# Kernel tuning notes

Measured on AMD Instinct MI355X. Metric: run time of the kernel, lower is better.

The kernel has to match this reference:

```python
import jax, jax.numpy as jnp
import numpy as np

# Dimensions (see shape_source): n_head == M == 8 is required by the module's own reshapes.
H = 8       # n_head
M = 8       # hardcoded M (must equal n_head)
D = 1024    # input_dim
E = 1024    # embed_dim
V = 128     # v_dim = embed_dim // n_head
KD = 128    # k_dim = v_dim
S = 10      # global seq_len == n_query (forced by delta_proj in-features)
K = 3       # K_num sampling points
HI, WI = 16, 16   # h_img, w_img feature-map size
BN = 4      # batch_n = batch_size // (h*w)
B = BN * HI * WI  # 1024
BNM = BN * M      # 32


def setup_inputs() -> dict:
    key = jax.random.key(0)
    ks = jax.random.split(key, 7)
    sc = 0.02
    return {
        "q": jax.random.normal(ks[0], (B, S, D), jnp.float32),
        "Wq": jax.random.normal(ks[1], (H, D, KD), jnp.float32) * sc,
        "Wk": jax.random.normal(ks[2], (H, D, KD), jnp.float32) * sc,
        "Wv": jax.random.normal(ks[3], (H, D, V * K), jnp.float32) * sc,
        "Wo": jax.random.normal(ks[4], (H, V, E), jnp.float32) * sc,
        "dw": jax.random.normal(ks[5], (2 * K * S, V * S), jnp.float32) * 0.01,
        "db": jax.random.uniform(ks[6], (2 * K * S,), jnp.float32, -1.0, 1.0),
    }


def _grid_sample_bilinear(feats, gx, gy):
    # Replicates F.grid_sample(mode='bilinear', padding_mode='zeros', align_corners=False)
    # feats: (N, h, w, S, V); gx, gy: (N, h, w, S, K) normalized grid coords in [-1, 1]-space
    n, h, w = feats.shape[0], feats.shape[1], feats.shape[2]
    ix = ((gx + 1.0) * w - 1.0) * 0.5  # unnormalize, align_corners=False
    iy = ((gy + 1.0) * h - 1.0) * 0.5
    x0 = jnp.floor(ix); y0 = jnp.floor(iy)
    x1 = x0 + 1.0;      y1 = y0 + 1.0
    wx1 = ix - x0; wx0 = 1.0 - wx1
    wy1 = iy - y0; wy0 = 1.0 - wy1
    b_idx = jnp.arange(n)[:, None, None, None, None]
    s_idx = jnp.arange(feats.shape[3])[None, None, None, :, None]

    def corner(xc, yc, wgt):
        xi = jnp.clip(xc.astype(jnp.int32), 0, w - 1)
        yi = jnp.clip(yc.astype(jnp.int32), 0, h - 1)
        valid = (xc >= 0) & (xc <= w - 1) & (yc >= 0) & (yc <= h - 1)
        val = feats[b_idx, yi, xi, s_idx]  # (N, h, w, S, K, V)
        return val * (wgt * valid)[..., None]

    return (corner(x0, y0, wx0 * wy0) + corner(x1, y0, wx1 * wy0)
            + corner(x0, y1, wx0 * wy1) + corner(x1, y1, wx1 * wy1))


def _l2norm_dim1(x):
    # F.normalize(x, p=2, dim=1) with eps=1e-12 (normalizes over the h axis)
    n = jnp.sqrt(jnp.sum(x * x, axis=1, keepdims=True))
    return x / jnp.maximum(n, 1e-12)


def _forward(q, Wq, Wk, Wv, Wo, dw, db):
    hf = q.reshape(-1, D)                                    # [B*S, D] (h defaults to q)
    qp = jnp.einsum('nd,hdk->hnk', hf, Wq).reshape(H, B, S, KD)
    kp = jnp.einsum('nd,hdk->hnk', hf, Wk).reshape(H, B, S, KD)
    vp = jnp.einsum('nd,hdk->hnk', hf, Wv).reshape(H, B, S * K, V)

    # torch: q.permute(1,2,3,0).contiguous().view(H, B, -1)  (memory reinterpretation)
    q2 = jnp.transpose(qp, (1, 2, 3, 0)).reshape(H, B, S * KD)

    deltas = (q2 @ dw.T + db).reshape(BNM, HI, WI, S, K, 2)

    gy, gx = jnp.meshgrid(jnp.arange(HI) / (HI - 1), jnp.arange(WI) / (WI - 1), indexing='ij')
    ref = jnp.stack((gx, gy), axis=-1).astype(q.dtype)        # (h, w, 2)

    pd = ref[None, :, :, None, None, :] + deltas              # (BNM, h, w, S, K, 2)
    vgx = _l2norm_dim1(pd[..., 0])
    vgy = _l2norm_dim1(pd[..., 1])

    feats = kp.reshape(BNM, HI, WI, S, V)                     # torch view of (H,B,S,k)
    samp = _grid_sample_bilinear(feats, vgx, vgy)             # (BNM, h, w, S, K, V)
    # torch stacks loop results at index k*S + s on a trailing dim, then permutes channels last
    samp = jnp.transpose(samp, (0, 1, 2, 4, 3, 5)).reshape(BNM, HI, WI, K * S, V)
    k_attn = samp.reshape(M, B, K * S, V)

    q_attn = q2.reshape(M, B, S, V)
    qk = jnp.einsum('mbqv,mbkv->mbqk', q_attn, k_attn) * (1.0 / np.sqrt(KD))
    attn = jax.nn.softmax(qk, axis=-1)                        # (M, B, S, K*S)
    attn_map = attn.mean(axis=0)[:, 0]                        # (B, K*S)

    head = jnp.einsum('mbqk,mbkv->mbqv', attn, vp)            # (M, B, S, V)
    head_flat = jnp.transpose(head, (1, 2, 0, 3)).reshape(B * S, H * V)
    out = (head_flat @ Wo.reshape(H * V, E)).reshape(B, S, E)
    return out, attn_map


def reference(q, Wq, Wk, Wv, Wo, dw, db):
    return _forward(q, Wq, Wk, Wv, Wo, dw, db)
```

## Files before the change

kernel.cpp:

```cpp
#include <hip/hip_runtime.h>


typedef float    f32x4 __attribute__((ext_vector_type(4)));
typedef short    s16x8 __attribute__((ext_vector_type(8)));
typedef unsigned short u16x8 __attribute__((ext_vector_type(8)));
typedef unsigned short u16;

__device__ __forceinline__ u16 f2bf(float f) {
  union { float f; unsigned u; } x; x.f = f;
  unsigned r = x.u + 0x7FFFu + ((x.u >> 16) & 1u);
  return (u16)(r >> 16);
}
__device__ __forceinline__ float bf2f(u16 u) {
  union { unsigned u; float f; } x; x.u = ((unsigned)u) << 16;
  return x.f;
}

#define ASYNC16(g, l) __builtin_amdgcn_global_load_lds(                       \
    (const __attribute__((address_space(1))) void*)(g),                       \
    (__attribute__((address_space(3))) void*)(l), 16, 0, 0)
#define WAITV(n) asm volatile("s_waitcnt vmcnt(" #n ")" ::: "memory")
#define WAITL    asm volatile("s_waitcnt lgkmcnt(0)" ::: "memory")
#define SB       __builtin_amdgcn_sched_barrier(0)
#define BAR      __builtin_amdgcn_s_barrier()

__global__ __launch_bounds__(256) void conv_all(
    const float* __restrict__ q, const float* __restrict__ Wq,
    const float* __restrict__ Wk, const float* __restrict__ Wv,
    const float* __restrict__ Wo, const float* __restrict__ dw,
    u16* __restrict__ Abf, u16* __restrict__ Wcat, u16* __restrict__ dwbf)
{
  int bid = blockIdx.x;
  if (bid < 5120) {
    int i = bid * 256 + threadIdx.x;
    const float4* s = (const float4*)q + (size_t)i * 2;
    float4 a = s[0], b = s[1];
    u16x8 o;
    o[0] = f2bf(a.x); o[1] = f2bf(a.y); o[2] = f2bf(a.z); o[3] = f2bf(a.w);
    o[4] = f2bf(b.x); o[5] = f2bf(b.y); o[6] = f2bf(b.z); o[7] = f2bf(b.w);
    *(u16x8*)(Abf + (size_t)i * 8) = o;
  } else if (bid < 8192) {
    int i = (bid - 5120) * 256 + threadIdx.x;
    int c = i >> 7;
    int d0 = (i & 127) * 8;
    const float* src; int stride;
    if (c < 1024)      { int kq = c >> 3, h = c & 7;
                         src = Wq + (size_t)h * 131072 + kq;      stride = 128; }
    else if (c < 2048) { int j = c - 1024; int h = j >> 7, k = j & 127;
                         src = Wk + (size_t)h * 131072 + k;       stride = 128; }
    else if (c < 5120) { int j = c - 2048; int h = j / 384, cc = j - h * 384;
                         src = Wv + (size_t)h * 393216 + cc;      stride = 384; }
    else               { int e = c - 5120;
                         src = Wo + e;                            stride = 1024; }
    u16x8 o;
#pragma unroll
    for (int r = 0; r < 8; ++r) o[r] = f2bf(src[(size_t)(d0 + r) * stride]);
    *(u16x8*)(Wcat + (size_t)c * 1024 + d0) = o;
  } else {
    int i = (bid - 8192) * 256 + threadIdx.x;
    if (i >= 10240) return;
    int row = i / 160, ch = i - row * 160;
    int srow = (row < 60) ? row : 0;
    const float4* s = (const float4*)(dw + (size_t)srow * 1280 + ch * 8);
    float4 a = s[0], b = s[1];
    u16x8 o;
    o[0] = f2bf(a.x); o[1] = f2bf(a.y); o[2] = f2bf(a.z); o[3] = f2bf(a.w);
    o[4] = f2bf(b.x); o[5] = f2bf(b.y); o[6] = f2bf(b.z); o[7] = f2bf(b.w);
    *(u16x8*)(dwbf + (size_t)row * 1280 + ch * 8) = o;
  }
}

__global__ __launch_bounds__(512, 2) void gemm_320(
    const u16* __restrict__ base, long bOff, u16* __restrict__ C, int ldc)
{
  extern __shared__ __align__(16) char smem[];
  const int tid = threadIdx.x;
  const int l   = tid & 63;
  const int wid = tid >> 6;
  const int wm  = wid >> 2;
  const int wn  = wid & 3;
  const int row0 = blockIdx.x * 320;
  const int col0 = blockIdx.y * 320;

  int eoff[5];
#pragma unroll
  for (int j = 0; j < 5; ++j) {
    int c = j * 512 + tid;
    int mc = (c < 1280) ? c : c - 1280;
    int rp = mc >> 3, s = mc & 7, gs = s ^ (rp & 7);
    int grow = rp * 2 + (gs >> 2), gk = (gs & 3) * 8;
    eoff[j] = (c < 1280) ? ((row0 + grow) * 1024 + gk)
                         : (int)(bOff + (size_t)(col0 + grow) * 1024 + gk);
  }

#define STG320(tt, bb) do {                                                   \
    _Pragma("unroll")                                                         \
    for (int j_ = 0; j_ < 5; ++j_)                                            \
      ASYNC16(base + eoff[j_] + (tt) * 32,                                    \
              smem + (bb) * 40960 + (j_ * 512 + tid) * 16);                   \
  } while (0)

  const int lrow = l & 15, lk = l >> 4;
  int aoff[10], boff[5];
  {
    int rowA = wm * 160 + lrow;
    int rpA = rowA >> 1, odA = (rowA & 1) << 2;
#pragma unroll
    for (int fm = 0; fm < 10; ++fm) {
      int rp = rpA + fm * 8;
      aoff[fm] = rp * 128 + (((odA | lk) ^ (rp & 7)) * 16);
    }
    int rowB = wn * 80 + lrow;
    int rpB = rowB >> 1, odB = (rowB & 1) << 2;
#pragma unroll
    for (int fn = 0; fn < 5; ++fn) {
      int rp = rpB + fn * 8;
      boff[fn] = 20480 + rp * 128 + (((odB | lk) ^ (rp & 7)) * 16);
    }
  }

  f32x4 acc[10][5];
#pragma unroll
  for (int i = 0; i < 10; ++i)
#pragma unroll
    for (int j = 0; j < 5; ++j) acc[i][j] = (f32x4){0.f, 0.f, 0.f, 0.f};

  STG320(0, 0); STG320(1, 1);
  WAITV(5);
  SB; BAR; SB;

  for (int t = 0; t < 32; ++t) {
    const int cb = t % 3;
    if (t + 2 < 32) STG320(t + 2, (t + 2) % 3);
    const char* Ab = smem + cb * 40960;
    s16x8 bR[5];
#pragma unroll
    for (int fn = 0; fn < 5; ++fn) bR[fn] = *(const s16x8*)(Ab + boff[fn]);
#pragma unroll
    for (int fm = 0; fm < 10; ++fm) {
      s16x8 aT = *(const s16x8*)(Ab + aoff[fm]);
#pragma unroll
      for (int fn = 0; fn < 5; ++fn)
        acc[fm][fn] = __builtin_amdgcn_mfma_f32_16x16x32_bf16(
            aT, bR[fn], acc[fm][fn], 0, 0, 0);
    }
    if (t + 2 < 32) { WAITV(5); }
    else if (t == 30) { WAITV(0); }
    SB; BAR; SB;
  }
#undef STG320

  const int crow = l >> 4, ccol = l & 15;
#pragma unroll
  for (int fm = 0; fm < 10; ++fm)
#pragma unroll
    for (int fn = 0; fn < 5; ++fn) {
      size_t rb = (size_t)(row0 + wm * 160 + fm * 16 + crow * 4);
      int col = col0 + wn * 80 + fn * 16 + ccol;
#pragma unroll
      for (int r = 0; r < 4; ++r)
        C[(rb + r) * ldc + col] = f2bf(acc[fm][fn][r]);
    }
}

template<int OUTBF>
__global__ __launch_bounds__(512, 2) void gemm_256(
    const u16* __restrict__ A, const u16* __restrict__ Bt,
    void* __restrict__ Cv, int ldc)
{
  extern __shared__ __align__(16) char smem[];
  const int tid = threadIdx.x;
  const int l   = tid & 63;
  const int wid = tid >> 6;
  const int wm  = wid >> 2;
  const int wn  = wid & 3;
  const int row0 = blockIdx.x * 256;
  const int col0 = blockIdx.y * 256;

  size_t goff[2]; int doff[2];
#pragma unroll
  for (int j = 0; j < 2; ++j) {
    int c = j * 512 + tid;
    int drow = c >> 3;
    int sg = (c & 7) ^ (drow & 7);
    goff[j] = (size_t)(drow * 2 + (sg >> 2)) * 1024 + (sg & 3) * 8;
    doff[j] = c * 16;
  }
  const u16* Agb = A  + (size_t)row0 * 1024;
  const u16* Bgb = Bt + (size_t)col0 * 1024;

#define STG(mtx, kh, tt, dd) do {                                             \
    const u16* sb_ = (mtx) ? Bgb : Agb;                                       \
    char* lb_ = smem + ((mtx) ? 65536 : 0) + (dd) * 32768 + (kh) * 16384;     \
    ASYNC16(sb_ + goff[0] + (tt) * 64 + (kh) * 32, lb_ + doff[0]);            \
    ASYNC16(sb_ + goff[1] + (tt) * 64 + (kh) * 32, lb_ + doff[1]);            \
  } while (0)

  const int lrow = l & 15, lk = l >> 4;
  const int p = (((lrow & 1) << 2) | lk) ^ ((lrow >> 1) & 7);
  const int rofs = (lrow >> 1) * 128 + p * 16;

  f32x4 acc[8][4];
#pragma unroll
  for (int i = 0; i < 8; ++i)
#pragma unroll
    for (int j = 0; j < 4; ++j) acc[i][j] = (f32x4){0.f, 0.f, 0.f, 0.f};

  STG(0, 0, 0, 0); STG(1, 0, 0, 0);
  STG(0, 1, 0, 0); STG(1, 1, 0, 0);
  WAITV(4);
  BAR; SB;

  for (int t = 0; t < 16; ++t) {
    const int d = t & 1;
    const char* Abase = smem + d * 32768;
    const char* Bbase = smem + 65536 + d * 32768;
    s16x8 aR[8], bR[4];

#pragma unroll
    for (int kh = 0; kh < 2; ++kh) {
      const char* Ab = Abase + kh * 16384 + wm * 8192;
      const char* Bb = Bbase + kh * 16384 + wn * 4096;
#pragma unroll
      for (int fm = 0; fm < 4; ++fm)
        aR[fm] = *(const s16x8*)(Ab + fm * 1024 + rofs);
#pragma unroll
      for (int fn = 0; fn < 4; ++fn)
        bR[fn] = *(const s16x8*)(Bb + fn * 1024 + rofs);
      if (t < 15) STG(0, kh, t + 1, d ^ 1);
      SB; BAR;
      WAITL; SB;
      __builtin_amdgcn_s_setprio(1);
#pragma unroll
      for (int fm = 0; fm < 4; ++fm)
#pragma unroll
        for (int fn = 0; fn < 4; ++fn)
          acc[fm][fn] = __builtin_amdgcn_mfma_f32_16x16x32_bf16(
              aR[fm], bR[fn], acc[fm][fn], 0, 0, 0);
      __builtin_amdgcn_s_setprio(0);
      SB; BAR;

#pragma unroll
      for (int fm = 4; fm < 8; ++fm)
        aR[fm] = *(const s16x8*)(Ab + fm * 1024 + rofs);
      if (t < 15) STG(1, kh, t + 1, d ^ 1);
      SB; BAR;
      WAITL; SB;
      __builtin_amdgcn_s_setprio(1);
#pragma unroll
      for (int fm = 4; fm < 8; ++fm)
#pragma unroll
        for (int fn = 0; fn < 4; ++fn)
          acc[fm][fn] = __builtin_amdgcn_mfma_f32_16x16x32_bf16(
              aR[fm], bR[fn], acc[fm][fn], 0, 0, 0);
      __builtin_amdgcn_s_setprio(0);
      if (kh == 0) {
        if (t == 15) WAITV(0); else WAITV(4);
      } else {
        if (t < 15) WAITV(4);
      }
      SB; BAR;
    }
  }
#undef STG

  const int crow = l >> 4, ccol = l & 15;
#pragma unroll
  for (int fm = 0; fm < 8; ++fm)
#pragma unroll
    for (int fn = 0; fn < 4; ++fn) {
      size_t rb = (size_t)(row0 + wm * 128 + fm * 16 + crow * 4);
      int col = col0 + wn * 64 + fn * 16 + ccol;
      if (OUTBF) {
        u16* Cq = (u16*)Cv;
#pragma unroll
        for (int r = 0; r < 4; ++r)
          Cq[(rb + r) * ldc + col] = f2bf(acc[fm][fn][r]);
      } else {
        float* Cf = (float*)Cv;
#pragma unroll
        for (int r = 0; r < 4; ++r)
          Cf[(rb + r) * ldc + col] = acc[fm][fn][r];
      }
    }
}

__global__ __launch_bounds__(256) void delta_mfma(
    const u16* __restrict__ proj, const u16* __restrict__ dwbf,
    const float* __restrict__ db, float* __restrict__ deltas)
{
  __shared__ __align__(16) u16 As[4][64 * 32];
  __shared__ __align__(16) u16 Bs[4][64 * 32];
  const int tid  = threadIdx.x;
  const int lane = tid & 63;
  const int w    = tid >> 6;
  const int row0 = blockIdx.x * 64;
  const int wr   = w * 16;
  const int lrow = lane & 15;
  const int lk   = lane >> 4;

  f32x4 acc[4];
#pragma unroll
  for (int j = 0; j < 4; ++j) acc[j] = (f32x4){0.f, 0.f, 0.f, 0.f};

  const size_t lin0 = (size_t)(row0 + (tid >> 2)) * 1280 + (tid & 3) * 8;
  const u16* Bg = dwbf + (size_t)(tid >> 2) * 1280 + (tid & 3) * 8;

#define STD(kk, bb) do {                                                      \
    size_t lin_ = lin0 + (kk) * 32;                                           \
    ASYNC16(proj + (lin_ >> 10) * 5120 + (lin_ & 1023),                       \
            (char*)As + (bb) * 4096 + w * 1024);                              \
    ASYNC16(Bg + (kk) * 32, (char*)Bs + (bb) * 4096 + w * 1024);              \
  } while (0)

  const int aoff = (wr + lrow) * 64 + lk * 16;
  int boff[4];
#pragma unroll
  for (int f = 0; f < 4; ++f) boff[f] = (f * 16 + lrow) * 64 + lk * 16;

  STD(0, 0); STD(1, 1); STD(2, 2);
  WAITV(4);
  SB; BAR; SB;

  for (int k = 0; k < 40; ++k) {
    const int bb = k & 3;
    if (k + 3 < 40) STD(k + 3, (k + 3) & 3);
    s16x8 af = *(const s16x8*)((const char*)As + bb * 4096 + aoff);
#pragma unroll
    for (int fn = 0; fn < 4; ++fn) {
      s16x8 bfr = *(const s16x8*)((const char*)Bs + bb * 4096 + boff[fn]);
      acc[fn] = __builtin_amdgcn_mfma_f32_16x16x32_bf16(af, bfr, acc[fn], 0, 0, 0);
    }
    if (k < 37)      { WAITV(4); }
    else if (k == 37){ WAITV(2); }
    else if (k == 38){ WAITV(0); }
    SB; BAR; SB;
  }
#undef STD

  const int crow = lane >> 4;
  const int ccol = lane & 15;
#pragma unroll
  for (int fn = 0; fn < 4; ++fn) {
    int col = fn * 16 + ccol;
    if (col < 60) {
      float d = db[col];
      size_t rb = (size_t)(row0 + wr + crow * 4);
#pragma unroll
      for (int r = 0; r < 4; ++r)
        deltas[(rb + r) * 60 + col] = acc[fn][r] + d;
    }
  }
}

__global__ void coords_kernel(const float* __restrict__ deltas,
                              float* __restrict__ vgx, float* __restrict__ vgy)
{
  int g = blockIdx.x * 256 + threadIdx.x;
  if (g >= 32 * 16 * 10 * 3) return;
  int kk = g % 3, tmp = g / 3;
  int s = tmp % 10; tmp /= 10;
  int wi = tmp % 16; int bnm = tmp / 16;
  float gxr = wi * (1.0f / 15.0f);
  float px[16], py[16];
  float sx = 0.f, sy = 0.f;
#pragma unroll
  for (int hi = 0; hi < 16; ++hi) {
    size_t base = ((size_t)((bnm * 16 + hi) * 16 + wi)) * 60 + (s * 3 + kk) * 2;
    float x = gxr + deltas[base];
    float y = hi * (1.0f / 15.0f) + deltas[base + 1];
    px[hi] = x; py[hi] = y;
    sx += x * x; sy += y * y;
  }
  float rx = 1.0f / fmaxf(sqrtf(sx), 1e-12f);
  float ry = 1.0f / fmaxf(sqrtf(sy), 1e-12f);
#pragma unroll
  for (int hi = 0; hi < 16; ++hi) {
    size_t o = ((size_t)((bnm * 16 + hi) * 16 + wi) * 10 + s) * 3 + kk;
    vgx[o] = px[hi] * rx;
    vgy[o] = py[hi] * ry;
  }
}

__global__ __launch_bounds__(256) void attn_mfma(
    const u16* __restrict__ proj, const float* __restrict__ vgx,
    const float* __restrict__ vgy, u16* __restrict__ headf,
    float* __restrict__ attn0)
{
  const int bid = blockIdx.x;
  const int m = bid >> 10, b = bid & 1023;
  const int tid = threadIdx.x;
  const int lane = tid & 63;
  const int w = tid >> 6;
  const int lr = lane & 15, g = lane >> 4;

  __shared__ __align__(16) u16 ksb[32][136];
  __shared__ __align__(16) u16 vt[128][32];
  __shared__ __align__(16) u16 pl[16][40];
  __shared__ float wst[30][4];
  __shared__ int   cst[30][4];

  s16x8 aq[4];
  {
    size_t linb = (size_t)bid * 1280 + (size_t)lr * 128 + (size_t)g * 8;
#pragma unroll
    for (int kk = 0; kk < 4; ++kk) {
      size_t lin = linb + kk * 32;
      aq[kk] = *(const s16x8*)(proj + (lin >> 10) * 5120 + (lin & 1023));
    }
  }

  if (tid < 30) {
    int t = tid, kk = t / 10, sk = t % 10;
    size_t ci = ((size_t)bid * 10 + sk) * 3 + kk;
    float gx = vgx[ci], gy = vgy[ci];
    float ix = (gx + 1.0f) * 8.0f - 0.5f;
    float iy = (gy + 1.0f) * 8.0f - 0.5f;
    float x0f = floorf(ix), y0f = floorf(iy);
    float wx1 = ix - x0f, wx0 = 1.0f - wx1;
    float wy1 = iy - y0f, wy0 = 1.0f - wy1;
    float x1f = x0f + 1.0f, y1f = y0f + 1.0f;
    bool vx0 = (x0f >= 0.f) && (x0f <= 15.f);
    bool vx1 = (x1f >= 0.f) && (x1f <= 15.f);
    bool vy0 = (y0f >= 0.f) && (y0f <= 15.f);
    bool vy1 = (y1f >= 0.f) && (y1f <= 15.f);
    int x0 = min(max((int)x0f, 0), 15);
    int x1 = min(max((int)x1f, 0), 15);
    int y0 = min(max((int)y0f, 0), 15);
    int y1 = min(max((int)y1f, 0), 15);
    wst[t][0] = wx0 * wy0 * ((vx0 && vy0) ? 1.f : 0.f);
    wst[t][1] = wx1 * wy0 * ((vx1 && vy0) ? 1.f : 0.f);
    wst[t][2] = wx0 * wy1 * ((vx0 && vy1) ? 1.f : 0.f);
    wst[t][3] = wx1 * wy1 * ((vx1 && vy1) ? 1.f : 0.f);
    cst[t][0] = x0; cst[t][1] = x1; cst[t][2] = y0; cst[t][3] = y1;
  }
  __syncthreads();

  for (int i = tid; i < 512; i += 256) {
    int t = i & 31, c = i >> 5;
    u16x8 v = (u16x8){0, 0, 0, 0, 0, 0, 0, 0};
    if (t < 30) {
      int sv = t / 3, cv = t - sv * 3;
      v = *(const u16x8*)(proj + ((size_t)(b * 10 + sv)) * 5120 + 2048 +
                          m * 384 + cv * 128 + c * 8);
    }
#pragma unroll
    for (int r = 0; r < 8; ++r)
      vt[8 * c + r][t ^ (8 * (r & 3))] = v[r];
  }

  {
    int pb = (b >> 8) << 8;
    for (int i = tid; i < 480; i += 256) {
      int t = i >> 4, c = i & 15;
      int sk = t % 10;
      int x0 = cst[t][0], x1 = cst[t][1], y0 = cst[t][2], y1 = cst[t][3];
      float w00 = wst[t][0], w10 = wst[t][1], w01 = wst[t][2], w11 = wst[t][3];
      size_t colo = 1024 + (size_t)m * 128 + c * 8;
      const u16x8 f00 = *(const u16x8*)&proj[((size_t)((pb + y0 * 16 + x0) * 10 + sk)) * 5120 + colo];
      const u16x8 f10 = *(const u16x8*)&proj[((size_t)((pb + y0 * 16 + x1) * 10 + sk)) * 5120 + colo];
      const u16x8 f01 = *(const u16x8*)&proj[((size_t)((pb + y1 * 16 + x0) * 10 + sk)) * 5120 + colo];
      const u16x8 f11 = *(const u16x8*)&proj[((size_t)((pb + y1 * 16 + x1) * 10 + sk)) * 5120 + colo];
      u16x8 o;
#pragma unroll
      for (int r = 0; r < 8; ++r) {
        float acc = w00 * bf2f(f00[r]) + w10 * bf2f(f10[r]) +
                    w01 * bf2f(f01[r]) + w11 * bf2f(f11[r]);
        o[r] = f2bf(acc);
      }
      *(u16x8*)&ksb[t][c * 8] = o;
    }
  }
  __syncthreads();

  f32x4 dq[2];
  dq[0] = (f32x4){0.f, 0.f, 0.f, 0.f};
  dq[1] = (f32x4){0.f, 0.f, 0.f, 0.f};
#pragma unroll
  for (int kk = 0; kk < 4; ++kk) {
    s16x8 b0 = *(const s16x8*)&ksb[lr][g * 8 + kk * 32];
    s16x8 b1 = *(const s16x8*)&ksb[16 + lr][g * 8 + kk * 32];
    dq[0] = __builtin_amdgcn_mfma_f32_16x16x32_bf16(aq[kk], b0, dq[0], 0, 0, 0);
    dq[1] = __builtin_amdgcn_mfma_f32_16x16x32_bf16(aq[kk], b1, dq[1], 0, 0, 0);
  }
  float p[2][4];
#pragma unroll
  for (int f = 0; f < 2; ++f) {
    int t = lr + 16 * f;
#pragma unroll
    for (int r = 0; r < 4; ++r) {
      float v = dq[f][r] * 0.08838834764831845f;
      p[f][r] = (t < 30) ? v : -1e30f;
    }
  }
#pragma unroll
  for (int r = 0; r < 4; ++r) {
    float mx = fmaxf(p[0][r], p[1][r]);
#pragma unroll
    for (int msk = 1; msk <= 8; msk <<= 1) mx = fmaxf(mx, __shfl_xor(mx, msk));
    float e0 = __expf(p[0][r] - mx);
    float e1 = __expf(p[1][r] - mx);
    float sm = e0 + e1;
#pragma unroll
    for (int msk = 1; msk <= 8; msk <<= 1) sm += __shfl_xor(sm, msk);
    float inv = 1.0f / sm;
    p[0][r] = e0 * inv;
    p[1][r] = e1 * inv;
  }
  if (w == 0 && g == 0) {
    attn0[(size_t)bid * 30 + lr] = p[0][0];
    if (lr < 14) attn0[(size_t)bid * 30 + 16 + lr] = p[1][0];
  }

#pragma unroll
  for (int f = 0; f < 2; ++f)
#pragma unroll
    for (int r = 0; r < 4; ++r)
      pl[g * 4 + r][lr + 16 * f] = f2bf(p[f][r]);
  WAITL; SB;

  s16x8 pa = *(const s16x8*)&pl[lr][g * 8];
#pragma unroll
  for (int qf = 0; qf < 2; ++qf) {
    int fv = w * 2 + qf;
    int v = fv * 16 + lr;
    s16x8 bv = *(const s16x8*)&vt[v][8 * (g ^ (v & 3))];
    f32x4 acc = (f32x4){0.f, 0.f, 0.f, 0.f};
    acc = __builtin_amdgcn_mfma_f32_16x16x32_bf16(pa, bv, acc, 0, 0, 0);
#pragma unroll
    for (int r = 0; r < 4; ++r) {
      int s = g * 4 + r;
      if (s < 10)
        headf[((size_t)(b * 10 + s)) * 1024 + m * 128 + v] = f2bf(acc[r]);
    }
  }
}

__global__ void attnmap_kernel(const float* __restrict__ attn0, float* __restrict__ outa)
{
  int i = blockIdx.x * 256 + threadIdx.x;
  if (i >= 30720) return;
  int b = i / 30, t = i % 30;
  float s = 0.f;
  for (int mm = 0; mm < 8; ++mm) s += attn0[((size_t)mm * 1024 + b) * 30 + t];
  outa[i] = 0.125f * s;
}

extern "C" void kernel_launch(void* const* d_in, const int* in_sizes, int n_in,
                              void* d_out, int out_size, void* d_ws, size_t ws_size,
                              hipStream_t stream)
{
  const float* q  = (const float*)d_in[0];
  const float* Wq = (const float*)d_in[1];
  const float* Wk = (const float*)d_in[2];
  const float* Wv = (const float*)d_in[3];
  const float* Wo = (const float*)d_in[4];
  const float* dw = (const float*)d_in[5];
  const float* db = (const float*)d_in[6];
  float* out = (float*)d_out;
  float* attn_out = out + 10485760;

  char* p = (char*)d_ws;
  u16*   Abf   = (u16*)p;   p += 20971520;
  u16*   Wcat  = (u16*)p;   p += 12582912;
  u16*   proj  = (u16*)p;   p += 104857600;
  u16*   headf = (u16*)p;   p += 20971520;
  u16*   dwbf  = (u16*)p;   p += 163840;
  float* dels  = (float*)p; p += 1966080;
  float* vgxp  = (float*)p; p += 983040;
  float* vgyp  = (float*)p; p += 983040;
  float* attn0 = (float*)p; p += 983040;

  conv_all<<<dim3(8232), dim3(256), 0, stream>>>(q, Wq, Wk, Wv, Wo, dw,
                                                 Abf, Wcat, dwbf);

  gemm_320<<<dim3(32, 16), dim3(512), 122880, stream>>>(
      Abf, 10485760L, proj, 5120);

  delta_mfma<<<dim3(128), dim3(256), 0, stream>>>(proj, dwbf, db, dels);
  coords_kernel<<<dim3(60), dim3(256), 0, stream>>>(dels, vgxp, vgyp);
  attn_mfma<<<dim3(8192), dim3(256), 0, stream>>>(proj, vgxp, vgyp, headf, attn0);
  attnmap_kernel<<<dim3(120), dim3(256), 0, stream>>>(attn0, attn_out);

  gemm_256<0><<<dim3(40, 4), dim3(512), 131072, stream>>>(
      headf, Wcat + (size_t)5120 * 1024, out, 1024);
}
```

Before: 249.9 us.

## Triple-buffer output GEMM with one barrier per k-step; single-wave softmax in attention

Rewrites the final output GEMM to a three-stage LDS ring that holds 32-wide k-tiles and issues loads two steps ahead. This replaces the old double buffer, which needed several barriers per step, with a single barrier per step, and cuts shared memory to 96KB. In the attention kernel, only wave 0 now computes QK and the softmax, since the other waves were computing the same values redundantly. A __syncthreads is added before the PV product. That removes duplicate work but adds a block-wide sync, and the other waves sit idle during the softmax.

```diff
diff --git a/kernel.cpp b/kernel.cpp
--- a/kernel.cpp
+++ b/kernel.cpp
@@ -163,10 +163,9 @@
     }
 }
 
-template<int OUTBF>
-__global__ __launch_bounds__(512, 2) void gemm_256(
+__global__ __launch_bounds__(512, 2) void gemm_256b(
     const u16* __restrict__ A, const u16* __restrict__ Bt,
-    void* __restrict__ Cv, int ldc)
+    float* __restrict__ C, int ldc)
 {
   extern __shared__ __align__(16) char smem[];
   const int tid = threadIdx.x;
@@ -177,28 +176,42 @@
   const int row0 = blockIdx.x * 256;
   const int col0 = blockIdx.y * 256;
 
-  size_t goff[2]; int doff[2];
-#pragma unroll
-  for (int j = 0; j < 2; ++j) {
+  const u16* gsrc[4];
+#pragma unroll
+  for (int j = 0; j < 4; ++j) {
     int c = j * 512 + tid;
-    int drow = c >> 3;
-    int sg = (c & 7) ^ (drow & 7);
-    goff[j] = (size_t)(drow * 2 + (sg >> 2)) * 1024 + (sg & 3) * 8;
-    doff[j] = c * 16;
-  }
-  const u16* Agb = A  + (size_t)row0 * 1024;
-  const u16* Bgb = Bt + (size_t)col0 * 1024;
-
-#define STG(mtx, kh, tt, dd) do {                                             \
-    const u16* sb_ = (mtx) ? Bgb : Agb;                                       \
-    char* lb_ = smem + ((mtx) ? 65536 : 0) + (dd) * 32768 + (kh) * 16384;     \
-    ASYNC16(sb_ + goff[0] + (tt) * 64 + (kh) * 32, lb_ + doff[0]);            \
-    ASYNC16(sb_ + goff[1] + (tt) * 64 + (kh) * 32, lb_ + doff[1]);            \
+    int mc = (c < 1024) ? c : c - 1024;
+    int rp = mc >> 3, s = mc & 7, gs = s ^ (rp & 7);
+    int grow = rp * 2 + (gs >> 2), gk = (gs & 3) * 8;
+    gsrc[j] = (c < 1024) ? (A + (size_t)(row0 + grow) * 1024 + gk)
+                         : (Bt + (size_t)(col0 + grow) * 1024 + gk);
+  }
+
+#define STG256(tt, bb) do {                                                   \
+    _Pragma("unroll")                                                         \
+    for (int j_ = 0; j_ < 4; ++j_)                                            \
+      ASYNC16(gsrc[j_] + (tt) * 32,                                           \
+              smem + (bb) * 32768 + (j_ * 512 + tid) * 16);                   \
   } while (0)
 
   const int lrow = l & 15, lk = l >> 4;
-  const int p = (((lrow & 1) << 2) | lk) ^ ((lrow >> 1) & 7);
-  const int rofs = (lrow >> 1) * 128 + p * 16;
+  int aoff[8], boff[4];
+  {
+    int rowA = wm * 128 + lrow;
+    int rpA = rowA >> 1, odA = (rowA & 1) << 2;
+#pragma unroll
+    for (int fm = 0; fm < 8; ++fm) {
+      int rp = rpA + fm * 8;
+      aoff[fm] = rp * 128 + (((odA | lk) ^ (rp & 7)) * 16);
+    }
+    int rowB = wn * 64 + lrow;
+    int rpB = rowB >> 1, odB = (rowB & 1) << 2;
+#pragma unroll
+    for (int fn = 0; fn < 4; ++fn) {
+      int rp = rpB + fn * 8;
+      boff[fn] = 16384 + rp * 128 + (((odB | lk) ^ (rp & 7)) * 16);
+    }
+  }
 
   f32x4 acc[8][4];
 #pragma unroll
@@ -206,63 +219,30 @@
 #pragma unroll
     for (int j = 0; j < 4; ++j) acc[i][j] = (f32x4){0.f, 0.f, 0.f, 0.f};
 
-  STG(0, 0, 0, 0); STG(1, 0, 0, 0);
-  STG(0, 1, 0, 0); STG(1, 1, 0, 0);
+  STG256(0, 0); STG256(1, 1);
   WAITV(4);
-  BAR; SB;
-
-  for (int t = 0; t < 16; ++t) {
-    const int d = t & 1;
-    const char* Abase = smem + d * 32768;
-    const char* Bbase = smem + 65536 + d * 32768;
-    s16x8 aR[8], bR[4];
-
-#pragma unroll
-    for (int kh = 0; kh < 2; ++kh) {
-      const char* Ab = Abase + kh * 16384 + wm * 8192;
-      const char* Bb = Bbase + kh * 16384 + wn * 4096;
-#pragma unroll
-      for (int fm = 0; fm < 4; ++fm)
-        aR[fm] = *(const s16x8*)(Ab + fm * 1024 + rofs);
+  SB; BAR; SB;
+
+  for (int t = 0; t < 32; ++t) {
+    const int cb = t % 3;
+    if (t + 2 < 32) STG256(t + 2, (t + 2) % 3);
+    const char* Ab = smem + cb * 32768;
+    s16x8 bR[4];
+#pragma unroll
+    for (int fn = 0; fn < 4; ++fn) bR[fn] = *(const s16x8*)(Ab + boff[fn]);
+#pragma unroll
+    for (int fm = 0; fm < 8; ++fm) {
+      s16x8 aT = *(const s16x8*)(Ab + aoff[fm]);
 #pragma unroll
       for (int fn = 0; fn < 4; ++fn)
-        bR[fn] = *(const s16x8*)(Bb + fn * 1024 + rofs);
-      if (t < 15) STG(0, kh, t + 1, d ^ 1);
-      SB; BAR;
-      WAITL; SB;
-      __builtin_amdgcn_s_setprio(1);
-#pragma unroll
-      for (int fm = 0; fm < 4; ++fm)
-#pragma unroll
-        for (int fn = 0; fn < 4; ++fn)
-          acc[fm][fn] = __builtin_amdgcn_mfma_f32_16x16x32_bf16(
-              aR[fm], bR[fn], acc[fm][fn], 0, 0, 0);
-      __builtin_amdgcn_s_setprio(0);
-      SB; BAR;
-
-#pragma unroll
-      for (int fm = 4; fm < 8; ++fm)
-        aR[fm] = *(const s16x8*)(Ab + fm * 1024 + rofs);
-      if (t < 15) STG(1, kh, t + 1, d ^ 1);
-      SB; BAR;
-      WAITL; SB;
-      __builtin_amdgcn_s_setprio(1);
-#pragma unroll
-      for (int fm = 4; fm < 8; ++fm)
-#pragma unroll
-        for (int fn = 0; fn < 4; ++fn)
-          acc[fm][fn] = __builtin_amdgcn_mfma_f32_16x16x32_bf16(
-              aR[fm], bR[fn], acc[fm][fn], 0, 0, 0);
-      __builtin_amdgcn_s_setprio(0);
-      if (kh == 0) {
-        if (t == 15) WAITV(0); else WAITV(4);
-      } else {
-        if (t < 15) WAITV(4);
-      }
-      SB; BAR;
-    }
-  }
-#undef STG
+        acc[fm][fn] = __builtin_amdgcn_mfma_f32_16x16x32_bf16(
+            aT, bR[fn], acc[fm][fn], 0, 0, 0);
+    }
+    if (t + 2 < 32) { WAITV(4); }
+    else if (t == 30) { WAITV(0); }
+    SB; BAR; SB;
+  }
+#undef STG256
 
   const int crow = l >> 4, ccol = l & 15;
 #pragma unroll
@@ -271,17 +251,9 @@
     for (int fn = 0; fn < 4; ++fn) {
       size_t rb = (size_t)(row0 + wm * 128 + fm * 16 + crow * 4);
       int col = col0 + wn * 64 + fn * 16 + ccol;
-      if (OUTBF) {
-        u16* Cq = (u16*)Cv;
-#pragma unroll
-        for (int r = 0; r < 4; ++r)
-          Cq[(rb + r) * ldc + col] = f2bf(acc[fm][fn][r]);
-      } else {
-        float* Cf = (float*)Cv;
-#pragma unroll
-        for (int r = 0; r < 4; ++r)
-          Cf[(rb + r) * ldc + col] = acc[fm][fn][r];
-      }
+#pragma unroll
+      for (int r = 0; r < 4; ++r)
+        C[(rb + r) * ldc + col] = acc[fm][fn][r];
     }
 }
 
@@ -392,7 +364,6 @@
   const int tid = threadIdx.x;
   const int lane = tid & 63;
   const int w = tid >> 6;
-  const int lr = lane & 15, g = lane >> 4;
 
   __shared__ __align__(16) u16 ksb[32][136];
   __shared__ __align__(16) u16 vt[128][32];
@@ -401,8 +372,8 @@
   __shared__ int   cst[30][4];
 
   s16x8 aq[4];
-  {
-    size_t linb = (size_t)bid * 1280 + (size_t)lr * 128 + (size_t)g * 8;
+  if (w == 0) {
+    size_t linb = (size_t)bid * 1280 + (size_t)(lane & 15) * 128 + (lane >> 4) * 8;
 #pragma unroll
     for (int kk = 0; kk < 4; ++kk) {
       size_t lin = linb + kk * 32;
@@ -473,52 +444,55 @@
   }
   __syncthreads();
 
-  f32x4 dq[2];
-  dq[0] = (f32x4){0.f, 0.f, 0.f, 0.f};
-  dq[1] = (f32x4){0.f, 0.f, 0.f, 0.f};
-#pragma unroll
-  for (int kk = 0; kk < 4; ++kk) {
-    s16x8 b0 = *(const s16x8*)&ksb[lr][g * 8 + kk * 32];
-    s16x8 b1 = *(const s16x8*)&ksb[16 + lr][g * 8 + kk * 32];
-    dq[0] = __builtin_amdgcn_mfma_f32_16x16x32_bf16(aq[kk], b0, dq[0], 0, 0, 0);
-    dq[1] = __builtin_amdgcn_mfma_f32_16x16x32_bf16(aq[kk], b1, dq[1], 0, 0, 0);
-  }
-  float p[2][4];
-#pragma unroll
-  for (int f = 0; f < 2; ++f) {
-    int t = lr + 16 * f;
+  if (w == 0) {
+    f32x4 dq[2];
+    dq[0] = (f32x4){0.f, 0.f, 0.f, 0.f};
+    dq[1] = (f32x4){0.f, 0.f, 0.f, 0.f};
+    const int lr = lane & 15, g = lane >> 4;
+#pragma unroll
+    for (int kk = 0; kk < 4; ++kk) {
+      s16x8 b0 = *(const s16x8*)&ksb[lr][g * 8 + kk * 32];
+      s16x8 b1 = *(const s16x8*)&ksb[16 + lr][g * 8 + kk * 32];
+      dq[0] = __builtin_amdgcn_mfma_f32_16x16x32_bf16(aq[kk], b0, dq[0], 0, 0, 0);
+      dq[1] = __builtin_amdgcn_mfma_f32_16x16x32_bf16(aq[kk], b1, dq[1], 0, 0, 0);
+    }
+    float p[2][4];
+#pragma unroll
+    for (int f = 0; f < 2; ++f) {
+      int t = lr + 16 * f;
+#pragma unroll
+      for (int r = 0; r < 4; ++r) {
+        float v = dq[f][r] * 0.08838834764831845f;
+        p[f][r] = (t < 30) ? v : -1e30f;
+      }
+    }
 #pragma unroll
     for (int r = 0; r < 4; ++r) {
-      float v = dq[f][r] * 0.08838834764831845f;
-      p[f][r] = (t < 30) ? v : -1e30f;
-    }
-  }
-#pragma unroll
-  for (int r = 0; r < 4; ++r) {
-    float mx = fmaxf(p[0][r], p[1][r]);
-#pragma unroll
-    for (int msk = 1; msk <= 8; msk <<= 1) mx = fmaxf(mx, __shfl_xor(mx, msk));
-    float e0 = __expf(p[0][r] - mx);
-    float e1 = __expf(p[1][r] - mx);
-    float sm = e0 + e1;
-#pragma unroll
-    for (int msk = 1; msk <= 8; msk <<= 1) sm += __shfl_xor(sm, msk);
-    float inv = 1.0f / sm;
-    p[0][r] = e0 * inv;
-    p[1][r] = e1 * inv;
-  }
-  if (w == 0 && g == 0) {
-    attn0[(size_t)bid * 30 + lr] = p[0][0];
-    if (lr < 14) attn0[(size_t)bid * 30 + 16 + lr] = p[1][0];
-  }
-
-#pragma unroll
-  for (int f = 0; f < 2; ++f)
-#pragma unroll
-    for (int r = 0; r < 4; ++r)
-      pl[g * 4 + r][lr + 16 * f] = f2bf(p[f][r]);
-  WAITL; SB;
-
+      float mx = fmaxf(p[0][r], p[1][r]);
+#pragma unroll
+      for (int msk = 1; msk <= 8; msk <<= 1) mx = fmaxf(mx, __shfl_xor(mx, msk));
+      float e0 = __expf(p[0][r] - mx);
+      float e1 = __expf(p[1][r] - mx);
+      float sm = e0 + e1;
+#pragma unroll
+      for (int msk = 1; msk <= 8; msk <<= 1) sm += __shfl_xor(sm, msk);
+      float inv = 1.0f / sm;
+      p[0][r] = e0 * inv;
+      p[1][r] = e1 * inv;
+    }
+    if (g == 0) {
+      attn0[(size_t)bid * 30 + lr] = p[0][0];
+      if (lr < 14) attn0[(size_t)bid * 30 + 16 + lr] = p[1][0];
+    }
+#pragma unroll
+    for (int f = 0; f < 2; ++f)
+#pragma unroll
+      for (int r = 0; r < 4; ++r)
+        pl[g * 4 + r][lr + 16 * f] = f2bf(p[f][r]);
+  }
+  __syncthreads();
+
+  const int lr = lane & 15, g = lane >> 4;
   s16x8 pa = *(const s16x8*)&pl[lr][g * 8];
 #pragma unroll
   for (int qf = 0; qf < 2; ++qf) {
@@ -582,6 +556,6 @@
   attn_mfma<<<dim3(8192), dim3(256), 0, stream>>>(proj, vgxp, vgyp, headf, attn0);
   attnmap_kernel<<<dim3(120), dim3(256), 0, stream>>>(attn0, attn_out);
 
-  gemm_256<0><<<dim3(40, 4), dim3(512), 131072, stream>>>(
+  gemm_256b<<<dim3(40, 4), dim3(512), 98304, stream>>>(
       headf, Wcat + (size_t)5120 * 1024, out, 1024);
 }
```

Measured after the change: 246.0 us. About the same (-1.5%).
